# Kernel optimization log

Hardware: AMD Instinct MI355X
Metric: run time of the kernel (lower is better)

## Reference

```python
import jax, jax.numpy as jnp
import numpy as np

C = 1024
HEAD = 128

def setup_inputs() -> dict:
    key = jax.random.key(0)
    kx, kq, kk, kv = jax.random.split(key, 4)
    x = jax.random.normal(kx, (8, 2048, C), dtype=jnp.float32)
    s = 1.0 / np.sqrt(C)
    Wq = jax.random.normal(kq, (C, HEAD), dtype=jnp.float32) * s
    Wk = jax.random.normal(kk, (C, HEAD), dtype=jnp.float32) * s
    Wv = jax.random.normal(kv, (C, HEAD), dtype=jnp.float32) * s
    return {"x": x, "Wq": Wq, "Wk": Wk, "Wv": Wv}

def reference(x, Wq, Wk, Wv):
    B, T, Cdim = x.shape
    q = jnp.einsum('btc,ch->bth', x, Wq)
    k = jnp.einsum('btc,ch->bth', x, Wk)
    v = jnp.einsum('btc,ch->bth', x, Wv)
    # scores scaled by C**-0.5 (faithful to source, which uses input width C)
    wei = jnp.einsum('bqh,bkh->bqk', q, k) * (Cdim ** -0.5)
    causal = jnp.tril(jnp.ones((T, T), dtype=bool))
    wei = jnp.where(causal, wei, -jnp.inf)
    wei = jax.nn.softmax(wei, axis=-1)
    # dropout p=0.0 -> identity
    return jnp.einsum('bqk,bkh->bqh', wei, v)
```

## Files before the change

### kernel.cpp

```cpp
#include <hip/hip_runtime.h>
#include <hip/hip_bf16.h>


typedef __attribute__((ext_vector_type(8))) short bf16x8;
typedef __attribute__((ext_vector_type(4))) float f32x4;

#define NB   8
#define TT   2048
#define CDIM 1024
#define HD   128
#define NTOK (NB * TT)
#define NW   384

using bf16 = __hip_bfloat16;

__device__ __forceinline__ short f2bs(float f) {
    unsigned u = __builtin_bit_cast(unsigned, f);
    return (short)((u + 0x7FFF + ((u >> 16) & 1)) >> 16);
}

__global__ __launch_bounds__(256) void prep_w_kernel(
        const float* __restrict__ Wq, const float* __restrict__ Wk,
        const float* __restrict__ Wv, bf16* __restrict__ Wp) {
    const int f  = blockIdx.x * 256 + threadIdx.x;
    const int l  = f & 63;
    const int nt = (f >> 6) % 24;
    const int sl = f / 1536;
    const int ln = l & 15, quad = l >> 4;
    const int n  = nt * 16 + ln;
    const int w  = n >> 7, h = n & 127;
    const float* W = (w == 0) ? Wq : (w == 1) ? Wk : Wv;
    const int k0 = sl * 32 + quad * 8;
    bf16x8 frag;
    #pragma unroll
    for (int j = 0; j < 8; j++)
        frag[j] = f2bs(W[(long)(k0 + j) * HD + h]);
    *(bf16x8*)((short*)Wp + (long)f * 8) = frag;
}

__global__ __launch_bounds__(512, 4) void qkv_proj_kernel(
        const float* __restrict__ x, const bf16* __restrict__ Wp,
        bf16* __restrict__ Q, bf16* __restrict__ Kp, bf16* __restrict__ Vp) {
    __shared__ __align__(16) short aLDS[2 * 32 * 64 * 8];
    const int tid  = threadIdx.x;
    const int wave = tid >> 6, lane = tid & 63;
    const int quad = lane >> 4, ln = lane & 15;
    const long mbase = (long)blockIdx.x * 32;

    #pragma unroll
    for (int j = 0; j < 8; j++) {
        const int fid = j * 512 + tid;
        const int fl  = fid & 63;
        const int fsl = (fid >> 6) & 31;
        const int fmt = fid >> 11;
        const float4* src = (const float4*)(
            x + (mbase + fmt * 16 + (fl & 15)) * CDIM + fsl * 32 + (fl >> 4) * 8);
        float4 u = src[0], v = src[1];
        bf16x8 fr;
        fr[0] = f2bs(u.x); fr[1] = f2bs(u.y); fr[2] = f2bs(u.z); fr[3] = f2bs(u.w);
        fr[4] = f2bs(v.x); fr[5] = f2bs(v.y); fr[6] = f2bs(v.z); fr[7] = f2bs(v.w);
        *(bf16x8*)(aLDS + (long)fid * 8) = fr;
    }
    __syncthreads();

    const f32x4 zero = {0.f, 0.f, 0.f, 0.f};
    f32x4 acc[2][3];
    #pragma unroll
    for (int mt = 0; mt < 2; mt++)
        #pragma unroll
        for (int nt = 0; nt < 3; nt++) acc[mt][nt] = zero;

    const short* a0 = aLDS + lane * 8;
    const short* bp = (const short*)Wp + (long)wave * 1536 + lane * 8;

    #pragma unroll 4
    for (int sl = 0; sl < 32; sl++) {
        bf16x8 af0 = *(const bf16x8*)(a0 + sl * 512);
        bf16x8 af1 = *(const bf16x8*)(a0 + 16384 + sl * 512);
        bf16x8 b0  = *(const bf16x8*)(bp + (long)sl * 12288);
        bf16x8 b1  = *(const bf16x8*)(bp + (long)sl * 12288 + 512);
        bf16x8 b2  = *(const bf16x8*)(bp + (long)sl * 12288 + 1024);
        acc[0][0] = __builtin_amdgcn_mfma_f32_16x16x32_bf16(af0, b0, acc[0][0], 0, 0, 0);
        acc[0][1] = __builtin_amdgcn_mfma_f32_16x16x32_bf16(af0, b1, acc[0][1], 0, 0, 0);
        acc[0][2] = __builtin_amdgcn_mfma_f32_16x16x32_bf16(af0, b2, acc[0][2], 0, 0, 0);
        acc[1][0] = __builtin_amdgcn_mfma_f32_16x16x32_bf16(af1, b0, acc[1][0], 0, 0, 0);
        acc[1][1] = __builtin_amdgcn_mfma_f32_16x16x32_bf16(af1, b1, acc[1][1], 0, 0, 0);
        acc[1][2] = __builtin_amdgcn_mfma_f32_16x16x32_bf16(af1, b2, acc[1][2], 0, 0, 0);
    }

    __syncthreads();
    short* kT = aLDS;
    short* vT = aLDS + 8192;

    #pragma unroll
    for (int mt = 0; mt < 2; mt++) {
        #pragma unroll
        for (int nt = 0; nt < 3; nt++) {
            const int n = wave * 48 + nt * 16 + ln;
            #pragma unroll
            for (int r = 0; r < 4; r++) {
                const int row = mt * 16 + quad * 4 + r;
                const short hv = f2bs(acc[mt][nt][r]);
                if (n < 128) {
                    long g = mbase + row;
                    int b = (int)(g >> 11), t = (int)(g & (TT - 1));
                    Q[((long)b * TT + t) * HD + n] = __builtin_bit_cast(bf16, hv);
                } else if (n < 256) {
                    kT[row * 136 + (n - 128)] = hv;
                } else {
                    vT[(n - 256) * 40 + row] = hv;
                }
            }
        }
    }
    __syncthreads();

    {
        const long tile = blockIdx.x;
        const int  kc = wave >> 1, ntk = wave & 1;
        bf16x8 kv = *(const bf16x8*)&kT[(ntk*16 + ln)*136 + kc*32 + quad*8];
        *(bf16x8*)((short*)Kp + (tile*8 + wave)*512 + lane*8) = kv;
        bf16x8 vv = *(const bf16x8*)&vT[(wave*16 + ln)*40 + quad*8];
        *(bf16x8*)((short*)Vp + (tile*8 + wave)*512 + lane*8) = vv;
    }
}

__global__ __launch_bounds__(256, 3) void attn_kernel(
        const bf16* __restrict__ Q, const bf16* __restrict__ Kp,
        const bf16* __restrict__ Vp, float* __restrict__ out) {
    __shared__ __align__(16) char smem[33024];

    const int tid  = threadIdx.x;
    const int wave = tid >> 6, lane = tid & 63;
    const int quad = lane >> 4, ln = lane & 15;
    const int b   = blockIdx.x & 7;
    const int idx = blockIdx.x >> 3;
    const int g   = idx >> 5, r_ = idx & 31;
    const int qi  = (g == 0) ? 127 - r_ : (g == 1) ? 64 + r_
                  : (g == 2) ? 63 - r_  : r_;
    const int qb  = qi * 16;
    const int ntiles = (qb + 16 + 31) >> 5;
    const int t0 = (ntiles * wave) >> 2;
    const int t1 = (ntiles * (wave + 1)) >> 2;

    const bf16* Qb  = Q + (long)b * TT * HD;
    const short* Kpb = (const short*)Kp + (long)b * 64 * 4096;
    const short* Vpb = (const short*)Vp + (long)b * 64 * 4096;

    short* pwave = (short*)smem + wave * 1280;

    bf16x8 qf[4];
    #pragma unroll
    for (int kc = 0; kc < 4; kc++)
        qf[kc] = *(const bf16x8*)(Qb + (long)(qb + ln)*HD + kc*32 + quad*8);

    const f32x4 zero = {0.f, 0.f, 0.f, 0.f};
    f32x4 o[8];
    #pragma unroll
    for (int ht = 0; ht < 8; ht++) o[ht] = zero;
    float li[4] = {0.f, 0.f, 0.f, 0.f};

    for (int kt = t0; kt < t1; ++kt) {
        const int j0 = kt * 32;
        const short* kbase = Kpb + (long)kt * 4096 + lane * 8;
        const short* vbase = Vpb + (long)kt * 4096 + lane * 8;
        bf16x8 kf[4][2];
        #pragma unroll
        for (int kc = 0; kc < 4; kc++)
            #pragma unroll
            for (int nt = 0; nt < 2; nt++)
                kf[kc][nt] = *(const bf16x8*)(kbase + (kc*2 + nt)*512);
        bf16x8 vf[8];
        #pragma unroll
        for (int ht = 0; ht < 8; ht++)
            vf[ht] = *(const bf16x8*)(vbase + ht*512);

        f32x4 s[2]; s[0] = zero; s[1] = zero;
        #pragma unroll
        for (int kc = 0; kc < 4; kc++) {
            s[0] = __builtin_amdgcn_mfma_f32_16x16x32_bf16(qf[kc], kf[kc][0], s[0], 0, 0, 0);
            s[1] = __builtin_amdgcn_mfma_f32_16x16x32_bf16(qf[kc], kf[kc][1], s[1], 0, 0, 0);
        }

        short* pb = pwave + (kt & 1) * 640;
        #pragma unroll
        for (int r = 0; r < 4; r++) {
            const int q = qb + quad*4 + r;
            #pragma unroll
            for (int nt = 0; nt < 2; nt++) {
                float p = __expf(s[nt][r] * 0.03125f);
                if (j0 + nt*16 + ln > q) p = 0.f;
                li[r] += p;
                pb[(quad*4 + r)*40 + nt*16 + ln] = f2bs(p);
            }
        }
        bf16x8 pf = *(const bf16x8*)&pb[ln*40 + quad*8];
        #pragma unroll
        for (int ht = 0; ht < 8; ht++)
            o[ht] = __builtin_amdgcn_mfma_f32_16x16x32_bf16(pf, vf[ht], o[ht], 0, 0, 0);
    }

    #pragma unroll
    for (int r = 0; r < 4; r++)
        #pragma unroll
        for (int d = 1; d < 16; d <<= 1) li[r] += __shfl_xor(li[r], d);

    __syncthreads();
    float* red  = (float*)smem;
    float* redl = (float*)(smem + 32768);
    #pragma unroll
    for (int ht = 0; ht < 8; ht++)
        #pragma unroll
        for (int r = 0; r < 4; r++)
            red[wave*2048 + (quad*4 + r)*128 + ht*16 + ln] = o[ht][r];
    if (ln == 0)
        #pragma unroll
        for (int r = 0; r < 4; r++) redl[wave*16 + quad*4 + r] = li[r];
    __syncthreads();

    {
        const int row = (tid * 8) >> 7, col = (tid * 8) & 127;
        const float lsum = redl[row] + redl[16 + row] + redl[32 + row] + redl[48 + row];
        float* op = out + ((long)b * TT + qb + row) * HD + col;
        #pragma unroll
        for (int j = 0; j < 8; j++) {
            float s = red[row*128 + col + j]        + red[2048 + row*128 + col + j]
                    + red[4096 + row*128 + col + j] + red[6144 + row*128 + col + j];
            op[j] = s / lsum;
        }
    }
}

extern "C" void kernel_launch(void* const* d_in, const int* in_sizes, int n_in,
                              void* d_out, int out_size, void* d_ws, size_t ws_size,
                              hipStream_t stream) {
    const float* x  = (const float*)d_in[0];
    const float* Wq = (const float*)d_in[1];
    const float* Wk = (const float*)d_in[2];
    const float* Wv = (const float*)d_in[3];
    float* outp = (float*)d_out;

    bf16* Wp = (bf16*)d_ws;
    bf16* Qm = Wp + (long)NW * CDIM;
    bf16* Kp = Qm + (long)NTOK * HD;
    bf16* Vp = Kp + (long)NTOK * HD;

    prep_w_kernel<<<192, 256, 0, stream>>>(Wq, Wk, Wv, Wp);
    qkv_proj_kernel<<<512, 512, 0, stream>>>(x, Wp, Qm, Kp, Vp);
    attn_kernel<<<NB * 128, 256, 0, stream>>>(Qm, Kp, Vp, outp);
}
```

Before: 144.1 us.

## Process 32 query rows per attention block to reuse K/V tiles

Each attention block now handles two 16-row query tiles (32 rows), so every K and V tile loaded from global memory feeds twice as many MFMAs. The grid halves to 512 blocks with a simpler two-group heavy/light ordering, and the per-block reduction across waves becomes a tree (pairwise, then final) with the output written straight from wave registers. Costs are higher register pressure (launch bounds lowered to 2 blocks per SIMD set), fewer blocks for load balancing, and extra syncthreads in the reduction.

```diff
diff --git a/kernel.cpp b/kernel.cpp
--- a/kernel.cpp
+++ b/kernel.cpp
@@ -125,7 +125,7 @@
     }
 }
 
-__global__ __launch_bounds__(256, 3) void attn_kernel(
+__global__ __launch_bounds__(256, 2) void attn_kernel(
         const bf16* __restrict__ Q, const bf16* __restrict__ Kp,
         const bf16* __restrict__ Vp, float* __restrict__ out) {
     __shared__ __align__(16) char smem[33024];
@@ -135,98 +135,155 @@
     const int quad = lane >> 4, ln = lane & 15;
     const int b   = blockIdx.x & 7;
     const int idx = blockIdx.x >> 3;
-    const int g   = idx >> 5, r_ = idx & 31;
-    const int qi  = (g == 0) ? 127 - r_ : (g == 1) ? 64 + r_
-                  : (g == 2) ? 63 - r_  : r_;
-    const int qb  = qi * 16;
-    const int ntiles = (qb + 16 + 31) >> 5;
+    const int qi  = (idx >> 5) ? (idx & 31) : 63 - (idx & 31);
+    const int qb  = qi * 32;
+    const int ntiles = qi + 1;
     const int t0 = (ntiles * wave) >> 2;
     const int t1 = (ntiles * (wave + 1)) >> 2;
 
-    const bf16* Qb  = Q + (long)b * TT * HD;
+    const bf16*  Qb  = Q + (long)b * TT * HD;
     const short* Kpb = (const short*)Kp + (long)b * 64 * 4096;
     const short* Vpb = (const short*)Vp + (long)b * 64 * 4096;
 
-    short* pwave = (short*)smem + wave * 1280;
-
-    bf16x8 qf[4];
-    #pragma unroll
-    for (int kc = 0; kc < 4; kc++)
-        qf[kc] = *(const bf16x8*)(Qb + (long)(qb + ln)*HD + kc*32 + quad*8);
+    short* pwave = (short*)smem + wave * 2560;
+
+    bf16x8 qf[2][4];
+    #pragma unroll
+    for (int mt = 0; mt < 2; mt++)
+        #pragma unroll
+        for (int kc = 0; kc < 4; kc++)
+            qf[mt][kc] = *(const bf16x8*)(Qb + (long)(qb + mt*16 + ln)*HD + kc*32 + quad*8);
 
     const f32x4 zero = {0.f, 0.f, 0.f, 0.f};
-    f32x4 o[8];
-    #pragma unroll
-    for (int ht = 0; ht < 8; ht++) o[ht] = zero;
-    float li[4] = {0.f, 0.f, 0.f, 0.f};
+    f32x4 o[2][8];
+    #pragma unroll
+    for (int mt = 0; mt < 2; mt++)
+        #pragma unroll
+        for (int ht = 0; ht < 8; ht++) o[mt][ht] = zero;
+    float li[2][4] = {{0.f,0.f,0.f,0.f},{0.f,0.f,0.f,0.f}};
 
     for (int kt = t0; kt < t1; ++kt) {
         const int j0 = kt * 32;
         const short* kbase = Kpb + (long)kt * 4096 + lane * 8;
-        const short* vbase = Vpb + (long)kt * 4096 + lane * 8;
         bf16x8 kf[4][2];
         #pragma unroll
         for (int kc = 0; kc < 4; kc++)
             #pragma unroll
             for (int nt = 0; nt < 2; nt++)
                 kf[kc][nt] = *(const bf16x8*)(kbase + (kc*2 + nt)*512);
+
+        f32x4 s[2][2];
+        s[0][0] = zero; s[0][1] = zero; s[1][0] = zero; s[1][1] = zero;
+        #pragma unroll
+        for (int kc = 0; kc < 4; kc++)
+            #pragma unroll
+            for (int mt = 0; mt < 2; mt++) {
+                s[mt][0] = __builtin_amdgcn_mfma_f32_16x16x32_bf16(qf[mt][kc], kf[kc][0], s[mt][0], 0, 0, 0);
+                s[mt][1] = __builtin_amdgcn_mfma_f32_16x16x32_bf16(qf[mt][kc], kf[kc][1], s[mt][1], 0, 0, 0);
+            }
+
+        short* pb = pwave + (kt & 1) * 1280;
+        #pragma unroll
+        for (int mt = 0; mt < 2; mt++)
+            #pragma unroll
+            for (int r = 0; r < 4; r++) {
+                const int q = qb + mt*16 + quad*4 + r;
+                #pragma unroll
+                for (int nt = 0; nt < 2; nt++) {
+                    float p = __expf(s[mt][nt][r] * 0.03125f);
+                    if (j0 + nt*16 + ln > q) p = 0.f;
+                    li[mt][r] += p;
+                    pb[(mt*16 + quad*4 + r)*40 + nt*16 + ln] = f2bs(p);
+                }
+            }
+
+        const short* vbase = Vpb + (long)kt * 4096 + lane * 8;
         bf16x8 vf[8];
         #pragma unroll
         for (int ht = 0; ht < 8; ht++)
             vf[ht] = *(const bf16x8*)(vbase + ht*512);
 
-        f32x4 s[2]; s[0] = zero; s[1] = zero;
-        #pragma unroll
-        for (int kc = 0; kc < 4; kc++) {
-            s[0] = __builtin_amdgcn_mfma_f32_16x16x32_bf16(qf[kc], kf[kc][0], s[0], 0, 0, 0);
-            s[1] = __builtin_amdgcn_mfma_f32_16x16x32_bf16(qf[kc], kf[kc][1], s[1], 0, 0, 0);
-        }
-
-        short* pb = pwave + (kt & 1) * 640;
-        #pragma unroll
-        for (int r = 0; r < 4; r++) {
-            const int q = qb + quad*4 + r;
-            #pragma unroll
-            for (int nt = 0; nt < 2; nt++) {
-                float p = __expf(s[nt][r] * 0.03125f);
-                if (j0 + nt*16 + ln > q) p = 0.f;
-                li[r] += p;
-                pb[(quad*4 + r)*40 + nt*16 + ln] = f2bs(p);
-            }
-        }
-        bf16x8 pf = *(const bf16x8*)&pb[ln*40 + quad*8];
-        #pragma unroll
-        for (int ht = 0; ht < 8; ht++)
-            o[ht] = __builtin_amdgcn_mfma_f32_16x16x32_bf16(pf, vf[ht], o[ht], 0, 0, 0);
-    }
-
-    #pragma unroll
-    for (int r = 0; r < 4; r++)
-        #pragma unroll
-        for (int d = 1; d < 16; d <<= 1) li[r] += __shfl_xor(li[r], d);
+        bf16x8 pf[2];
+        #pragma unroll
+        for (int mt = 0; mt < 2; mt++)
+            pf[mt] = *(const bf16x8*)&pb[(mt*16 + ln)*40 + quad*8];
+        #pragma unroll
+        for (int mt = 0; mt < 2; mt++)
+            #pragma unroll
+            for (int ht = 0; ht < 8; ht++)
+                o[mt][ht] = __builtin_amdgcn_mfma_f32_16x16x32_bf16(pf[mt], vf[ht], o[mt][ht], 0, 0, 0);
+    }
+
+    #pragma unroll
+    for (int mt = 0; mt < 2; mt++)
+        #pragma unroll
+        for (int r = 0; r < 4; r++)
+            #pragma unroll
+            for (int d = 1; d < 16; d <<= 1) li[mt][r] += __shfl_xor(li[mt][r], d);
 
     __syncthreads();
     float* red  = (float*)smem;
     float* redl = (float*)(smem + 32768);
-    #pragma unroll
-    for (int ht = 0; ht < 8; ht++)
-        #pragma unroll
-        for (int r = 0; r < 4; r++)
-            red[wave*2048 + (quad*4 + r)*128 + ht*16 + ln] = o[ht][r];
-    if (ln == 0)
-        #pragma unroll
-        for (int r = 0; r < 4; r++) redl[wave*16 + quad*4 + r] = li[r];
-    __syncthreads();
-
-    {
-        const int row = (tid * 8) >> 7, col = (tid * 8) & 127;
-        const float lsum = redl[row] + redl[16 + row] + redl[32 + row] + redl[48 + row];
-        float* op = out + ((long)b * TT + qb + row) * HD + col;
-        #pragma unroll
-        for (int j = 0; j < 8; j++) {
-            float s = red[row*128 + col + j]        + red[2048 + row*128 + col + j]
-                    + red[4096 + row*128 + col + j] + red[6144 + row*128 + col + j];
-            op[j] = s / lsum;
+    if (wave & 1) {
+        const int slot = wave >> 1;
+        #pragma unroll
+        for (int mt = 0; mt < 2; mt++)
+            #pragma unroll
+            for (int ht = 0; ht < 8; ht++)
+                #pragma unroll
+                for (int r = 0; r < 4; r++)
+                    red[slot*4096 + (mt*16 + quad*4 + r)*128 + ht*16 + ln] = o[mt][ht][r];
+        if (ln == 0)
+            #pragma unroll
+            for (int mt = 0; mt < 2; mt++)
+                #pragma unroll
+                for (int r = 0; r < 4; r++)
+                    redl[slot*32 + mt*16 + quad*4 + r] = li[mt][r];
+    }
+    __syncthreads();
+    if (!(wave & 1)) {
+        const int slot = wave >> 1;
+        #pragma unroll
+        for (int mt = 0; mt < 2; mt++) {
+            #pragma unroll
+            for (int ht = 0; ht < 8; ht++)
+                #pragma unroll
+                for (int r = 0; r < 4; r++)
+                    o[mt][ht][r] += red[slot*4096 + (mt*16 + quad*4 + r)*128 + ht*16 + ln];
+            #pragma unroll
+            for (int r = 0; r < 4; r++)
+                li[mt][r] += redl[slot*32 + mt*16 + quad*4 + r];
+        }
+    }
+    __syncthreads();
+    if (wave == 2) {
+        #pragma unroll
+        for (int mt = 0; mt < 2; mt++) {
+            #pragma unroll
+            for (int ht = 0; ht < 8; ht++)
+                #pragma unroll
+                for (int r = 0; r < 4; r++)
+                    red[(mt*16 + quad*4 + r)*128 + ht*16 + ln] = o[mt][ht][r];
+            if (ln == 0)
+                #pragma unroll
+                for (int r = 0; r < 4; r++)
+                    redl[mt*16 + quad*4 + r] = li[mt][r];
+        }
+    }
+    __syncthreads();
+    if (wave == 0) {
+        #pragma unroll
+        for (int mt = 0; mt < 2; mt++) {
+            #pragma unroll
+            for (int r = 0; r < 4; r++)
+                li[mt][r] += redl[mt*16 + quad*4 + r];
+            #pragma unroll
+            for (int ht = 0; ht < 8; ht++)
+                #pragma unroll
+                for (int r = 0; r < 4; r++) {
+                    float v = o[mt][ht][r] + red[(mt*16 + quad*4 + r)*128 + ht*16 + ln];
+                    out[((long)b*TT + qb + mt*16 + quad*4 + r)*HD + ht*16 + ln] = v / li[mt][r];
+                }
         }
     }
 }
@@ -247,5 +304,5 @@
 
     prep_w_kernel<<<192, 256, 0, stream>>>(Wq, Wk, Wv, Wp);
     qkv_proj_kernel<<<512, 512, 0, stream>>>(x, Wp, Qm, Kp, Vp);
-    attn_kernel<<<NB * 128, 256, 0, stream>>>(Qm, Kp, Vp, outp);
-}
+    attn_kernel<<<NB * 64, 256, 0, stream>>>(Qm, Kp, Vp, outp);
+}
```

Result: no change. 143.2 us (-0.6%).
